# Optimization experiments

Hardware: AMD Instinct MI355X
Metric: run time of the kernel (lower is better)

## Reference

```python
import jax, jax.numpy as jnp
import numpy as np

B, C, H, W = 8, 256, 128, 128


def setup_inputs() -> dict:
    key = jax.random.key(0)
    k1, k2, k3, k4, k5 = jax.random.split(key, 5)
    x = jax.random.normal(k1, (B, C, H, W), dtype=jnp.float32)
    # 1x1 conv weights stored as (out_channels, in_channels); bias (out_channels,)
    w1 = jax.random.normal(k2, (C, C), dtype=jnp.float32) * (1.0 / np.sqrt(C))
    b1 = jax.random.normal(k3, (C,), dtype=jnp.float32) * 0.01
    w2 = jax.random.normal(k4, (C, C), dtype=jnp.float32) * (1.0 / np.sqrt(C))
    b2 = jax.random.normal(k5, (C,), dtype=jnp.float32) * 0.01
    return {"x": x, "w1": w1, "b1": b1, "w2": w2, "b2": b2}


def reference(x, w1, b1, w2, b2):
    b, c, h, w = x.shape
    xf = x.reshape(b, c, h * w)                      # (B, C, N)
    # 1x1 convs == per-pixel linear maps over channels
    q = jnp.einsum('oc,bcn->bon', w1, xf) + b1[None, :, None]   # (B, C, N)
    k = jnp.einsum('oc,bcn->bon', w2, xf) + b2[None, :, None]   # (B, C, N)
    # channel-attention Gram matrix: (B, C, N) @ (B, N, C) -> (B, C, C)
    attention = jnp.einsum('bcn,bdn->bcd', q, k)
    attention = jax.nn.softmax(attention, axis=-1)
    # (B, C, C) @ (B, C, N) -> (B, C, N), v = x itself (unprojected)
    attention_v = jnp.einsum('bcd,bdn->bcn', attention, xf).reshape(b, c, h, w)
    return x + attention_v
```

## Files before the change

### kernel.cpp

```cpp
#include <hip/hip_runtime.h>
#include <hip/hip_bf16.h>

#define B_    8
#define C_    256
#define NPIX  16384
#define BK    64
#define KC4   16
#define KCH4  (NPIX / KC4)
#define NSTEP4 (KCH4 / BK)

typedef __attribute__((ext_vector_type(8))) short bf16x8;
typedef __attribute__((ext_vector_type(4))) float f32x4;
typedef unsigned int uint_;

__device__ __forceinline__ unsigned short f2bf(float x) {
  unsigned int u = __builtin_bit_cast(unsigned int, x);
  u = (u + 0x7fffu + ((u >> 16) & 1u)) >> 16;
  return (unsigned short)u;
}
__device__ __forceinline__ float fcomp(const float4& v, int i) {
  switch (i) { case 0: return v.x; case 1: return v.y; case 2: return v.z; default: return v.w; }
}

template<bool XBF>
__global__ __launch_bounds__(512, 2) void k_gram(const float* __restrict__ x,
                                                 float* __restrict__ gpart,
                                                 float* __restrict__ spart,
                                                 unsigned short* __restrict__ xbf) {
  const int bid  = blockIdx.x;
  const int half = bid >> 7;
  const int b    = (bid >> 4) & 7;
  const int kc   = bid & 15;
  const float* X = x + (size_t)b * C_ * NPIX + kc * KCH4;

  __shared__ __align__(16) unsigned short Hi[2][256 * 64];
  __shared__ __align__(16) unsigned short Lo[2][256 * 64];

  const int tid  = threadIdx.x;
  const int lane = tid & 63;
  const int w    = tid >> 6;
  const int wr   = w >> 2;
  const int wc   = w & 3;

  const int srow = tid >> 4;
  const int scol = (tid & 15) * 4;
  const float* sp = X + (size_t)srow * NPIX + scol;
  unsigned short* xrow = XBF ?
      (xbf + (size_t)b * C_ * NPIX + (size_t)srow * NPIX + kc * KCH4 + scol) : nullptr;

  float rs[8] = {};
  float4 g[8];

#define GLOAD(ks)                                                             \
  _Pragma("unroll")                                                           \
  for (int j = 0; j < 8; ++j)                                                 \
    g[j] = *reinterpret_cast<const float4*>(sp + (size_t)j * 32 * NPIX + (ks) * BK);

#define STAGE(buf, ksn)                                                       \
  _Pragma("unroll")                                                           \
  for (int j = 0; j < 8; ++j) {                                               \
    const float4 v = g[j];                                                    \
    rs[j] += (v.x + v.y) + (v.z + v.w);                                       \
    const uint_ u0 = __builtin_bit_cast(uint_, v.x);                          \
    const uint_ u1 = __builtin_bit_cast(uint_, v.y);                          \
    const uint_ u2 = __builtin_bit_cast(uint_, v.z);                          \
    const uint_ u3 = __builtin_bit_cast(uint_, v.w);                          \
    uint2 hi, lo;                                                             \
    hi.x = (u0 >> 16) | (u1 & 0xffff0000u);                                   \
    hi.y = (u2 >> 16) | (u3 & 0xffff0000u);                                   \
    const float h0 = __builtin_bit_cast(float, u0 & 0xffff0000u);             \
    const float h1 = __builtin_bit_cast(float, u1 & 0xffff0000u);             \
    const float h2 = __builtin_bit_cast(float, u2 & 0xffff0000u);             \
    const float h3 = __builtin_bit_cast(float, u3 & 0xffff0000u);             \
    const uint_ l0 = __builtin_bit_cast(uint_, v.x - h0);                     \
    const uint_ l1 = __builtin_bit_cast(uint_, v.y - h1);                     \
    const uint_ l2 = __builtin_bit_cast(uint_, v.z - h2);                     \
    const uint_ l3 = __builtin_bit_cast(uint_, v.w - h3);                     \
    lo.x = (l0 >> 16) | (l1 & 0xffff0000u);                                   \
    lo.y = (l2 >> 16) | (l3 & 0xffff0000u);                                   \
    const int row = j * 32 + srow;                                            \
    const int idx = (row * 64 + scol) ^ ((row & 7) << 3);                     \
    *reinterpret_cast<uint2*>(&Hi[buf][idx]) = hi;                            \
    *reinterpret_cast<uint2*>(&Lo[buf][idx]) = lo;                            \
    if (XBF && (j >> 2) == half)                                              \
      *reinterpret_cast<uint2*>(xrow + (size_t)j * 32 * NPIX + (ksn) * BK) = hi; \
  }

  GLOAD(0)
  STAGE(0, 0)
  __syncthreads();

  f32x4 acc[4][4] = {};

  for (int ks = 0; ks < NSTEP4; ++ks) {
    const int cur = ks & 1;
    if (ks + 1 < NSTEP4) GLOAD(ks + 1)
    __builtin_amdgcn_s_setprio(1);
#pragma unroll
    for (int kk = 0; kk < 2; ++kk) {
      const int kb = kk * 32 + (lane >> 4) * 8;
      bf16x8 ahi[4], bhi[4], blo[4];
#pragma unroll
      for (int m = 0; m < 4; ++m) {
        const int row = half * 128 + wr * 64 + m * 16 + (lane & 15);
        ahi[m] = *reinterpret_cast<const bf16x8*>(&Hi[cur][(row * 64 + kb) ^ ((row & 7) << 3)]);
      }
#pragma unroll
      for (int n = 0; n < 4; ++n) {
        const int row = wc * 64 + n * 16 + (lane & 15);
        bhi[n] = *reinterpret_cast<const bf16x8*>(&Hi[cur][(row * 64 + kb) ^ ((row & 7) << 3)]);
      }
#pragma unroll
      for (int m = 0; m < 4; ++m)
#pragma unroll
        for (int n = 0; n < 4; ++n)
          acc[m][n] = __builtin_amdgcn_mfma_f32_16x16x32_bf16(ahi[m], bhi[n], acc[m][n], 0, 0, 0);
#pragma unroll
      for (int n = 0; n < 4; ++n) {
        const int row = wc * 64 + n * 16 + (lane & 15);
        blo[n] = *reinterpret_cast<const bf16x8*>(&Lo[cur][(row * 64 + kb) ^ ((row & 7) << 3)]);
      }
#pragma unroll
      for (int m = 0; m < 4; ++m)
#pragma unroll
        for (int n = 0; n < 4; ++n)
          acc[m][n] = __builtin_amdgcn_mfma_f32_16x16x32_bf16(ahi[m], blo[n], acc[m][n], 0, 0, 0);
#pragma unroll
      for (int m = 0; m < 4; ++m) {
        const int row = half * 128 + wr * 64 + m * 16 + (lane & 15);
        bf16x8 alo = *reinterpret_cast<const bf16x8*>(&Lo[cur][(row * 64 + kb) ^ ((row & 7) << 3)]);
#pragma unroll
        for (int n = 0; n < 4; ++n)
          acc[m][n] = __builtin_amdgcn_mfma_f32_16x16x32_bf16(alo, bhi[n], acc[m][n], 0, 0, 0);
      }
    }
    __builtin_amdgcn_s_setprio(0);
    if (ks + 1 < NSTEP4) STAGE(cur ^ 1, ks + 1)
    __syncthreads();
  }
#undef GLOAD
#undef STAGE

#pragma unroll
  for (int j = 0; j < 8; ++j) {
#pragma unroll
    for (int off = 1; off < 16; off <<= 1) rs[j] += __shfl_xor(rs[j], off, 64);
  }
  if (half == 0 && (tid & 15) == 0) {
#pragma unroll
    for (int j = 0; j < 8; ++j)
      spart[((size_t)b * KC4 + kc) * 256 + j * 32 + srow] = rs[j];
  }

  float* gp = gpart + (size_t)bid * (128 * 256);
#pragma unroll
  for (int m = 0; m < 4; ++m) {
    const int row0 = wr * 64 + m * 16 + ((lane >> 4) << 2);
#pragma unroll
    for (int n = 0; n < 4; ++n) {
      const int col = wc * 64 + n * 16 + (lane & 15);
#pragma unroll
      for (int j = 0; j < 4; ++j)
        gp[(size_t)(row0 + j) * 256 + col] = acc[m][n][j];
    }
  }
}

__global__ __launch_bounds__(256) void k_reduce(const float* __restrict__ gpart,
                                                float* __restrict__ G) {
  const int t  = blockIdx.x * 256 + threadIdx.x;
  const int b  = t >> 14;
  const int i  = (t >> 6) & 255;
  const int j4 = (t & 63) * 4;
  const int hb = (i >> 7) * 128 + b * 16;
  const int il = i & 127;
  float4 s = make_float4(0.f, 0.f, 0.f, 0.f);
#pragma unroll
  for (int kc = 0; kc < KC4; ++kc) {
    const float4 v = *reinterpret_cast<const float4*>(
        &gpart[(size_t)(hb + kc) * (128 * 256) + (size_t)il * 256 + j4]);
    s.x += v.x; s.y += v.y; s.z += v.z; s.w += v.w;
  }
  *reinterpret_cast<float4*>(&G[((size_t)b * 256 + i) * 256 + j4]) = s;
}

__global__ __launch_bounds__(256) void k_transpose(const float* __restrict__ in,
                                                   float* __restrict__ outp) {
  __shared__ float t[32][33];
  const int bx = blockIdx.x & 7, by = blockIdx.x >> 3;
  const int tx = threadIdx.x & 31, ty = threadIdx.x >> 5;
#pragma unroll
  for (int i = 0; i < 32; i += 8)
    t[ty + i][tx] = in[(size_t)(by * 32 + ty + i) * 256 + bx * 32 + tx];
  __syncthreads();
#pragma unroll
  for (int i = 0; i < 32; i += 8)
    outp[(size_t)(bx * 32 + ty + i) * 256 + by * 32 + tx] = t[tx][ty + i];
}

__global__ __launch_bounds__(256) void k_u(const float* __restrict__ w1,
                                           const float* __restrict__ w2,
                                           const float* __restrict__ spart,
                                           float* __restrict__ u1,
                                           float* __restrict__ u2) {
  const int b = blockIdx.x;
  const int tid = threadIdx.x;
  __shared__ float sl[256];
  float sv = 0.f;
#pragma unroll
  for (int kc = 0; kc < KC4; ++kc) sv += spart[((size_t)b * KC4 + kc) * 256 + tid];
  sl[tid] = sv;
  __syncthreads();
  float a1 = 0.f, a2 = 0.f;
#pragma unroll 4
  for (int c = 0; c < 256; ++c) {
    a1 += w1[(size_t)tid * 256 + c] * sl[c];
    a2 += w2[(size_t)tid * 256 + c] * sl[c];
  }
  u1[b * 256 + tid] = a1;
  u2[b * 256 + tid] = a2;
}

__global__ __launch_bounds__(256) void k_smallmm(const float* __restrict__ A, long asb,
                                                 const float* __restrict__ Bm, long bsb,
                                                 float* __restrict__ Cm, long csb) {
  const int b  = blockIdx.y;
  const int i0 = blockIdx.x * 8;
  const float* Ab = A  + (size_t)asb * b;
  const float* Bb = Bm + (size_t)bsb * b;
  float*       Cb = Cm + (size_t)csb * b;
  const int tid = threadIdx.x;
  __shared__ float arows[8][256];
#pragma unroll
  for (int rr = 0; rr < 8; ++rr) arows[rr][tid] = Ab[(size_t)(i0 + rr) * 256 + tid];
  __syncthreads();
  float acc[8] = {};
#pragma unroll 4
  for (int k = 0; k < 256; ++k) {
    const float bv = Bb[(size_t)k * 256 + tid];
#pragma unroll
    for (int rr = 0; rr < 8; ++rr) acc[rr] += arows[rr][k] * bv;
  }
#pragma unroll
  for (int rr = 0; rr < 8; ++rr) Cb[(size_t)(i0 + rr) * 256 + tid] = acc[rr];
}

__global__ __launch_bounds__(256) void k_softmax(const float* __restrict__ L,
                                                 const float* __restrict__ b1,
                                                 const float* __restrict__ b2,
                                                 const float* __restrict__ u1,
                                                 const float* __restrict__ u2,
                                                 unsigned short* __restrict__ Abf) {
  const int b = blockIdx.y, i = blockIdx.x, j = threadIdx.x;
  const size_t base = ((size_t)b * 256 + i) * 256;
  const float v = L[base + j] + u1[b * 256 + i] * b2[j] +
                  b1[i] * (u2[b * 256 + j] + 16384.f * b2[j]);
  const int lane = j & 63, wv = j >> 6;
  __shared__ float redm[4], reds[4];
  float m = v;
#pragma unroll
  for (int off = 32; off; off >>= 1) m = fmaxf(m, __shfl_xor(m, off, 64));
  if (lane == 0) redm[wv] = m;
  __syncthreads();
  m = fmaxf(fmaxf(redm[0], redm[1]), fmaxf(redm[2], redm[3]));
  const float e = __expf(v - m);
  float sm = e;
#pragma unroll
  for (int off = 32; off; off >>= 1) sm += __shfl_xor(sm, off, 64);
  if (lane == 0) reds[wv] = sm;
  __syncthreads();
  sm = (reds[0] + reds[1]) + (reds[2] + reds[3]);
  float p = e / sm;
  if (j == i) p += 1.0f;
  Abf[base + j] = f2bf(p);
}

template<bool XBF>
__global__ __launch_bounds__(256, 4) void k_av(const unsigned short* __restrict__ Abf,
                                               const float* __restrict__ x,
                                               const unsigned short* __restrict__ xbf,
                                               float* __restrict__ out) {
  const int bid = blockIdx.x;
  const int b = bid & 7;
  const int nbase = (bid >> 3) * 32;
  const unsigned short* Ab = Abf + (size_t)b * 65536;
  float* Ob = out + (size_t)b * C_ * NPIX;

  __shared__ __align__(16) unsigned short Xt[32 * 256];

  const int tid = threadIdx.x;
  const int lane = tid & 63, w = tid >> 6;

  if (XBF) {
    const unsigned short* Xh = xbf + (size_t)b * C_ * NPIX;
    const int pq = (tid & 7) * 4;
    const int dq = (tid >> 3) * 4;
#pragma unroll
    for (int h = 0; h < 2; ++h) {
      const int d = dq + h * 128;
      const unsigned short* xs = Xh + (size_t)d * NPIX + nbase + pq;
      ushort4 r0 = *reinterpret_cast<const ushort4*>(xs);
      ushort4 r1 = *reinterpret_cast<const ushort4*>(xs + NPIX);
      ushort4 r2 = *reinterpret_cast<const ushort4*>(xs + 2 * NPIX);
      ushort4 r3 = *reinterpret_cast<const ushort4*>(xs + 3 * NPIX);
      const ushort4 rr[4] = {r0, r1, r2, r3};
#pragma unroll
      for (int i = 0; i < 4; ++i) {
        const int px = pq + i;
        ushort4 v = make_ushort4(((const unsigned short*)&rr[0])[i],
                                 ((const unsigned short*)&rr[1])[i],
                                 ((const unsigned short*)&rr[2])[i],
                                 ((const unsigned short*)&rr[3])[i]);
        const int idx = (px * 256 + d) ^ (((px ^ (px >> 2)) & 7) << 3);
        *reinterpret_cast<ushort4*>(&Xt[idx]) = v;
      }
    }
  } else {
    const float* Xb = x + (size_t)b * C_ * NPIX;
    const int pq = (tid & 7) * 4;
    const int dq = (tid >> 3) * 4;
#pragma unroll
    for (int h = 0; h < 2; ++h) {
      const int d = dq + h * 128;
      const float* xs = Xb + (size_t)d * NPIX + nbase + pq;
      const float4 r0 = *reinterpret_cast<const float4*>(xs);
      const float4 r1 = *reinterpret_cast<const float4*>(xs + NPIX);
      const float4 r2 = *reinterpret_cast<const float4*>(xs + 2 * NPIX);
      const float4 r3 = *reinterpret_cast<const float4*>(xs + 3 * NPIX);
#pragma unroll
      for (int i = 0; i < 4; ++i) {
        const int px = pq + i;
        ushort4 v = make_ushort4(f2bf(fcomp(r0, i)), f2bf(fcomp(r1, i)),
                                 f2bf(fcomp(r2, i)), f2bf(fcomp(r3, i)));
        const int idx = (px * 256 + d) ^ (((px ^ (px >> 2)) & 7) << 3);
        *reinterpret_cast<ushort4*>(&Xt[idx]) = v;
      }
    }
  }
  __syncthreads();

  const int kboff = (lane >> 4) * 8;
  f32x4 acc[4][2] = {};
  bf16x8 afA[4], afB[4], bq[2];

#define LOADA(kk, af)                                                         \
  _Pragma("unroll")                                                           \
  for (int m = 0; m < 4; ++m)                                                 \
    af[m] = *reinterpret_cast<const bf16x8*>(                                 \
        Ab + (size_t)(w * 64 + m * 16 + (lane & 15)) * 256 + (kk) * 32 + kboff);

#define LOADB(kk)                                                             \
  _Pragma("unroll")                                                           \
  for (int n = 0; n < 2; ++n) {                                               \
    const int px = n * 16 + (lane & 15);                                      \
    bq[n] = *reinterpret_cast<const bf16x8*>(                                 \
        &Xt[(px * 256 + (kk) * 32 + kboff) ^ (((px ^ (px >> 2)) & 7) << 3)]); \
  }

#define MFMA8(af)                                                             \
  _Pragma("unroll")                                                           \
  for (int m = 0; m < 4; ++m)                                                 \
    _Pragma("unroll")                                                         \
    for (int n = 0; n < 2; ++n)                                               \
      acc[m][n] = __builtin_amdgcn_mfma_f32_16x16x32_bf16(bq[n], af[m], acc[m][n], 0, 0, 0);

  LOADA(0, afA)
#pragma unroll
  for (int kk = 0; kk < 8; ++kk) {
    LOADB(kk)
    if (kk < 7) {
      if (kk & 1) { LOADA(kk + 1, afA) } else { LOADA(kk + 1, afB) }
    }
    if (kk & 1) { MFMA8(afB) } else { MFMA8(afA) }
  }
#undef LOADA
#undef LOADB
#undef MFMA8

#pragma unroll
  for (int m = 0; m < 4; ++m) {
    const int ch = w * 64 + m * 16 + (lane & 15);
    float* orow = Ob + (size_t)ch * NPIX + nbase;
#pragma unroll
    for (int n = 0; n < 2; ++n) {
      const int p0 = n * 16 + ((lane >> 4) << 2);
      *reinterpret_cast<float4*>(orow + p0) = *reinterpret_cast<const float4*>(&acc[m][n]);
    }
  }
}

extern "C" void kernel_launch(void* const* d_in, const int* in_sizes, int n_in,
                              void* d_out, int out_size, void* d_ws, size_t ws_size,
                              hipStream_t stream) {
  const float* x  = (const float*)d_in[0];
  const float* w1 = (const float*)d_in[1];
  const float* b1 = (const float*)d_in[2];
  const float* w2 = (const float*)d_in[3];
  const float* b2 = (const float*)d_in[4];
  float* out = (float*)d_out;
  char* ws = (char*)d_ws;

  float* gpart = out;

  constexpr size_t G_OFF     = 0;
  constexpr size_t T1_OFF    = G_OFF   + (size_t)B_ * C_ * C_ * 4;
  constexpr size_t L_OFF     = T1_OFF  + (size_t)B_ * C_ * C_ * 4;
  constexpr size_t W2T_OFF   = L_OFF   + (size_t)B_ * C_ * C_ * 4;
  constexpr size_t SPART_OFF = W2T_OFF + (size_t)C_ * C_ * 4;
  constexpr size_t U1_OFF    = SPART_OFF + (size_t)B_ * KC4 * C_ * 4;
  constexpr size_t U2_OFF    = U1_OFF  + (size_t)B_ * C_ * 4;
  constexpr size_t ABF_OFF   = U2_OFF  + (size_t)B_ * C_ * 4;
  constexpr size_t XBF_OFF   = ABF_OFF + (size_t)B_ * C_ * C_ * 2;
  constexpr size_t XBF_BYTES = (size_t)B_ * C_ * NPIX * 2;

  float* G     = (float*)(ws + G_OFF);
  float* T1    = (float*)(ws + T1_OFF);
  float* Lb    = (float*)(ws + L_OFF);
  float* w2t   = (float*)(ws + W2T_OFF);
  float* spart = (float*)(ws + SPART_OFF);
  float* u1    = (float*)(ws + U1_OFF);
  float* u2    = (float*)(ws + U2_OFF);
  unsigned short* Abf = (unsigned short*)(ws + ABF_OFF);
  unsigned short* Xbf = (unsigned short*)(ws + XBF_OFF);

  const bool xbf_ok = ws_size >= XBF_OFF + XBF_BYTES;

  k_transpose<<<64, 256, 0, stream>>>(w2, w2t);
  if (xbf_ok) k_gram<true> <<<256, 512, 0, stream>>>(x, gpart, spart, Xbf);
  else        k_gram<false><<<256, 512, 0, stream>>>(x, gpart, spart, nullptr);
  k_reduce   <<<512, 256, 0, stream>>>(gpart, G);
  k_u        <<<B_, 256, 0, stream>>>(w1, w2, spart, u1, u2);
  k_smallmm  <<<dim3(32, B_), 256, 0, stream>>>(w1, 0, G, C_ * C_, T1, C_ * C_);
  k_smallmm  <<<dim3(32, B_), 256, 0, stream>>>(T1, C_ * C_, w2t, 0, Lb, C_ * C_);
  k_softmax  <<<dim3(C_, B_), 256, 0, stream>>>(Lb, b1, b2, u1, u2, Abf);
  if (xbf_ok) k_av<true> <<<4096, 256, 0, stream>>>(Abf, x, Xbf, out);
  else        k_av<false><<<4096, 256, 0, stream>>>(Abf, x, nullptr, out);
}
```

Before: 220.5 us.

## Split Gram K-dimension into 32 chunks and single-buffer LDS staging

Doubles the number of K-chunks in the Gram kernel, so the grid grows from 256 to 512 blocks and the per-block LDS shrinks from double-buffered to single-buffered. Staging now happens at the top of each iteration behind a barrier, with the next global load issued before the MFMA work. The goal is to fill more CUs and lift occupancy on a chip with 256 CUs. The cost is twice as many partial Gram tiles written and reduced, and less overlap between LDS staging and compute.

After: 254.9 us. 15.6% more time.

```diff
diff --git a/kernel.cpp b/kernel.cpp
--- a/kernel.cpp
+++ b/kernel.cpp
@@ -5,9 +5,9 @@
 #define C_    256
 #define NPIX  16384
 #define BK    64
-#define KC4   16
-#define KCH4  (NPIX / KC4)
-#define NSTEP4 (KCH4 / BK)
+#define KCG   32
+#define KCHG  (NPIX / KCG)
+#define NSTEPG (KCHG / BK)
 
 typedef __attribute__((ext_vector_type(8))) short bf16x8;
 typedef __attribute__((ext_vector_type(4))) float f32x4;
@@ -23,18 +23,18 @@
 }
 
 template<bool XBF>
-__global__ __launch_bounds__(512, 2) void k_gram(const float* __restrict__ x,
-                                                 float* __restrict__ gpart,
-                                                 float* __restrict__ spart,
-                                                 unsigned short* __restrict__ xbf) {
+__global__ __launch_bounds__(512) void k_gram(const float* __restrict__ x,
+                                              float* __restrict__ gpart,
+                                              float* __restrict__ spart,
+                                              unsigned short* __restrict__ xbf) {
   const int bid  = blockIdx.x;
-  const int half = bid >> 7;
-  const int b    = (bid >> 4) & 7;
-  const int kc   = bid & 15;
-  const float* X = x + (size_t)b * C_ * NPIX + kc * KCH4;
-
-  __shared__ __align__(16) unsigned short Hi[2][256 * 64];
-  __shared__ __align__(16) unsigned short Lo[2][256 * 64];
+  const int half = bid >> 8;
+  const int b    = (bid >> 5) & 7;
+  const int kc   = bid & 31;
+  const float* X = x + (size_t)b * C_ * NPIX + kc * KCHG;
+
+  __shared__ __align__(16) unsigned short Hi[256 * 64];
+  __shared__ __align__(16) unsigned short Lo[256 * 64];
 
   const int tid  = threadIdx.x;
   const int lane = tid & 63;
@@ -46,7 +46,7 @@
   const int scol = (tid & 15) * 4;
   const float* sp = X + (size_t)srow * NPIX + scol;
   unsigned short* xrow = XBF ?
-      (xbf + (size_t)b * C_ * NPIX + (size_t)srow * NPIX + kc * KCH4 + scol) : nullptr;
+      (xbf + (size_t)b * C_ * NPIX + (size_t)srow * NPIX + kc * KCHG + scol) : nullptr;
 
   float rs[8] = {};
   float4 g[8];
@@ -56,7 +56,7 @@
   for (int j = 0; j < 8; ++j)                                                 \
     g[j] = *reinterpret_cast<const float4*>(sp + (size_t)j * 32 * NPIX + (ks) * BK);
 
-#define STAGE(buf, ksn)                                                       \
+#define STAGE(ksn)                                                            \
   _Pragma("unroll")                                                           \
   for (int j = 0; j < 8; ++j) {                                               \
     const float4 v = g[j];                                                    \
@@ -80,21 +80,20 @@
     lo.y = (l2 >> 16) | (l3 & 0xffff0000u);                                   \
     const int row = j * 32 + srow;                                            \
     const int idx = (row * 64 + scol) ^ ((row & 7) << 3);                     \
-    *reinterpret_cast<uint2*>(&Hi[buf][idx]) = hi;                            \
-    *reinterpret_cast<uint2*>(&Lo[buf][idx]) = lo;                            \
+    *reinterpret_cast<uint2*>(&Hi[idx]) = hi;                                 \
+    *reinterpret_cast<uint2*>(&Lo[idx]) = lo;                                 \
     if (XBF && (j >> 2) == half)                                              \
       *reinterpret_cast<uint2*>(xrow + (size_t)j * 32 * NPIX + (ksn) * BK) = hi; \
   }
 
   GLOAD(0)
-  STAGE(0, 0)
-  __syncthreads();
 
   f32x4 acc[4][4] = {};
 
-  for (int ks = 0; ks < NSTEP4; ++ks) {
-    const int cur = ks & 1;
-    if (ks + 1 < NSTEP4) GLOAD(ks + 1)
+  for (int ks = 0; ks < NSTEPG; ++ks) {
+    STAGE(ks)
+    __syncthreads();
+    if (ks + 1 < NSTEPG) GLOAD(ks + 1)
     __builtin_amdgcn_s_setprio(1);
 #pragma unroll
     for (int kk = 0; kk < 2; ++kk) {
@@ -103,12 +102,12 @@
 #pragma unroll
       for (int m = 0; m < 4; ++m) {
         const int row = half * 128 + wr * 64 + m * 16 + (lane & 15);
-        ahi[m] = *reinterpret_cast<const bf16x8*>(&Hi[cur][(row * 64 + kb) ^ ((row & 7) << 3)]);
+        ahi[m] = *reinterpret_cast<const bf16x8*>(&Hi[(row * 64 + kb) ^ ((row & 7) << 3)]);
       }
 #pragma unroll
       for (int n = 0; n < 4; ++n) {
         const int row = wc * 64 + n * 16 + (lane & 15);
-        bhi[n] = *reinterpret_cast<const bf16x8*>(&Hi[cur][(row * 64 + kb) ^ ((row & 7) << 3)]);
+        bhi[n] = *reinterpret_cast<const bf16x8*>(&Hi[(row * 64 + kb) ^ ((row & 7) << 3)]);
       }
 #pragma unroll
       for (int m = 0; m < 4; ++m)
@@ -118,7 +117,7 @@
 #pragma unroll
       for (int n = 0; n < 4; ++n) {
         const int row = wc * 64 + n * 16 + (lane & 15);
-        blo[n] = *reinterpret_cast<const bf16x8*>(&Lo[cur][(row * 64 + kb) ^ ((row & 7) << 3)]);
+        blo[n] = *reinterpret_cast<const bf16x8*>(&Lo[(row * 64 + kb) ^ ((row & 7) << 3)]);
       }
 #pragma unroll
       for (int m = 0; m < 4; ++m)
@@ -128,14 +127,13 @@
 #pragma unroll
       for (int m = 0; m < 4; ++m) {
         const int row = half * 128 + wr * 64 + m * 16 + (lane & 15);
-        bf16x8 alo = *reinterpret_cast<const bf16x8*>(&Lo[cur][(row * 64 + kb) ^ ((row & 7) << 3)]);
+        bf16x8 alo = *reinterpret_cast<const bf16x8*>(&Lo[(row * 64 + kb) ^ ((row & 7) << 3)]);
 #pragma unroll
         for (int n = 0; n < 4; ++n)
           acc[m][n] = __builtin_amdgcn_mfma_f32_16x16x32_bf16(alo, bhi[n], acc[m][n], 0, 0, 0);
       }
     }
     __builtin_amdgcn_s_setprio(0);
-    if (ks + 1 < NSTEP4) STAGE(cur ^ 1, ks + 1)
     __syncthreads();
   }
 #undef GLOAD
@@ -149,7 +147,7 @@
   if (half == 0 && (tid & 15) == 0) {
 #pragma unroll
     for (int j = 0; j < 8; ++j)
-      spart[((size_t)b * KC4 + kc) * 256 + j * 32 + srow] = rs[j];
+      spart[((size_t)b * KCG + kc) * 256 + j * 32 + srow] = rs[j];
   }
 
   float* gp = gpart + (size_t)bid * (128 * 256);
@@ -172,11 +170,11 @@
   const int b  = t >> 14;
   const int i  = (t >> 6) & 255;
   const int j4 = (t & 63) * 4;
-  const int hb = (i >> 7) * 128 + b * 16;
+  const int hb = (i >> 7) * 256 + b * 32;
   const int il = i & 127;
   float4 s = make_float4(0.f, 0.f, 0.f, 0.f);
 #pragma unroll
-  for (int kc = 0; kc < KC4; ++kc) {
+  for (int kc = 0; kc < KCG; ++kc) {
     const float4 v = *reinterpret_cast<const float4*>(
         &gpart[(size_t)(hb + kc) * (128 * 256) + (size_t)il * 256 + j4]);
     s.x += v.x; s.y += v.y; s.z += v.z; s.w += v.w;
@@ -208,7 +206,7 @@
   __shared__ float sl[256];
   float sv = 0.f;
 #pragma unroll
-  for (int kc = 0; kc < KC4; ++kc) sv += spart[((size_t)b * KC4 + kc) * 256 + tid];
+  for (int kc = 0; kc < KCG; ++kc) sv += spart[((size_t)b * KCG + kc) * 256 + tid];
   sl[tid] = sv;
   __syncthreads();
   float a1 = 0.f, a2 = 0.f;
@@ -407,7 +405,7 @@
   constexpr size_t L_OFF     = T1_OFF  + (size_t)B_ * C_ * C_ * 4;
   constexpr size_t W2T_OFF   = L_OFF   + (size_t)B_ * C_ * C_ * 4;
   constexpr size_t SPART_OFF = W2T_OFF + (size_t)C_ * C_ * 4;
-  constexpr size_t U1_OFF    = SPART_OFF + (size_t)B_ * KC4 * C_ * 4;
+  constexpr size_t U1_OFF    = SPART_OFF + (size_t)B_ * KCG * C_ * 4;
   constexpr size_t U2_OFF    = U1_OFF  + (size_t)B_ * C_ * 4;
   constexpr size_t ABF_OFF   = U2_OFF  + (size_t)B_ * C_ * 4;
   constexpr size_t XBF_OFF   = ABF_OFF + (size_t)B_ * C_ * C_ * 2;
@@ -426,8 +424,8 @@
   const bool xbf_ok = ws_size >= XBF_OFF + XBF_BYTES;
 
   k_transpose<<<64, 256, 0, stream>>>(w2, w2t);
-  if (xbf_ok) k_gram<true> <<<256, 512, 0, stream>>>(x, gpart, spart, Xbf);
-  else        k_gram<false><<<256, 512, 0, stream>>>(x, gpart, spart, nullptr);
+  if (xbf_ok) k_gram<true> <<<512, 512, 0, stream>>>(x, gpart, spart, Xbf);
+  else        k_gram<false><<<512, 512, 0, stream>>>(x, gpart, spart, nullptr);
   k_reduce   <<<512, 256, 0, stream>>>(gpart, G);
   k_u        <<<B_, 256, 0, stream>>>(w1, w2, spart, u1, u2);
   k_smallmm  <<<dim3(32, B_), 256, 0, stream>>>(w1, 0, G, C_ * C_, T1, C_ * C_);
```

## Make k_av persistent over four pixel tiles with double-buffered LDS prefetch

Applied to the files above, without the earlier changes.

Each k_av block now handles four 32-pixel tiles instead of one, so the grid shrinks from 4096 to 1024 blocks. The next tile's X values are prefetched from global into registers while MFMAs run on the current tile, using a double-buffered LDS transpose. MFMA sections are wrapped in s_setprio. This is meant to hide global load latency and cut per-block launch overhead, at the cost of more registers (the occupancy hint in launch_bounds is dropped), double the LDS, and fewer blocks to spread across CUs.

Result: slower. 225.9 us (+2.5%).

```diff
diff --git a/kernel.cpp b/kernel.cpp
--- a/kernel.cpp
+++ b/kernel.cpp
@@ -276,72 +276,70 @@
 }
 
 template<bool XBF>
-__global__ __launch_bounds__(256, 4) void k_av(const unsigned short* __restrict__ Abf,
-                                               const float* __restrict__ x,
-                                               const unsigned short* __restrict__ xbf,
-                                               float* __restrict__ out) {
+__global__ __launch_bounds__(256) void k_av(const unsigned short* __restrict__ Abf,
+                                            const float* __restrict__ x,
+                                            const unsigned short* __restrict__ xbf,
+                                            float* __restrict__ out) {
   const int bid = blockIdx.x;
   const int b = bid & 7;
-  const int nbase = (bid >> 3) * 32;
+  const int pxbase = (bid >> 3) * 128;
   const unsigned short* Ab = Abf + (size_t)b * 65536;
   float* Ob = out + (size_t)b * C_ * NPIX;
 
-  __shared__ __align__(16) unsigned short Xt[32 * 256];
+  __shared__ __align__(16) unsigned short Xt[2][32 * 256];
 
   const int tid = threadIdx.x;
   const int lane = tid & 63, w = tid >> 6;
-
-  if (XBF) {
-    const unsigned short* Xh = xbf + (size_t)b * C_ * NPIX;
-    const int pq = (tid & 7) * 4;
-    const int dq = (tid >> 3) * 4;
-#pragma unroll
-    for (int h = 0; h < 2; ++h) {
-      const int d = dq + h * 128;
-      const unsigned short* xs = Xh + (size_t)d * NPIX + nbase + pq;
-      ushort4 r0 = *reinterpret_cast<const ushort4*>(xs);
-      ushort4 r1 = *reinterpret_cast<const ushort4*>(xs + NPIX);
-      ushort4 r2 = *reinterpret_cast<const ushort4*>(xs + 2 * NPIX);
-      ushort4 r3 = *reinterpret_cast<const ushort4*>(xs + 3 * NPIX);
-      const ushort4 rr[4] = {r0, r1, r2, r3};
-#pragma unroll
-      for (int i = 0; i < 4; ++i) {
-        const int px = pq + i;
-        ushort4 v = make_ushort4(((const unsigned short*)&rr[0])[i],
-                                 ((const unsigned short*)&rr[1])[i],
-                                 ((const unsigned short*)&rr[2])[i],
-                                 ((const unsigned short*)&rr[3])[i]);
-        const int idx = (px * 256 + d) ^ (((px ^ (px >> 2)) & 7) << 3);
-        *reinterpret_cast<ushort4*>(&Xt[idx]) = v;
-      }
-    }
-  } else {
-    const float* Xb = x + (size_t)b * C_ * NPIX;
-    const int pq = (tid & 7) * 4;
-    const int dq = (tid >> 3) * 4;
-#pragma unroll
-    for (int h = 0; h < 2; ++h) {
-      const int d = dq + h * 128;
-      const float* xs = Xb + (size_t)d * NPIX + nbase + pq;
-      const float4 r0 = *reinterpret_cast<const float4*>(xs);
-      const float4 r1 = *reinterpret_cast<const float4*>(xs + NPIX);
-      const float4 r2 = *reinterpret_cast<const float4*>(xs + 2 * NPIX);
-      const float4 r3 = *reinterpret_cast<const float4*>(xs + 3 * NPIX);
-#pragma unroll
-      for (int i = 0; i < 4; ++i) {
-        const int px = pq + i;
-        ushort4 v = make_ushort4(f2bf(fcomp(r0, i)), f2bf(fcomp(r1, i)),
-                                 f2bf(fcomp(r2, i)), f2bf(fcomp(r3, i)));
-        const int idx = (px * 256 + d) ^ (((px ^ (px >> 2)) & 7) << 3);
-        *reinterpret_cast<ushort4*>(&Xt[idx]) = v;
-      }
-    }
-  }
-  __syncthreads();
-
+  const int pq = (tid & 7) * 4;
+  const int dq = (tid >> 3) * 4;
   const int kboff = (lane >> 4) * 8;
-  f32x4 acc[4][2] = {};
-  bf16x8 afA[4], afB[4], bq[2];
+
+  const unsigned short* Xh = XBF ? (xbf + (size_t)b * C_ * NPIX) : nullptr;
+  const float*          Xf = XBF ? nullptr : (x + (size_t)b * C_ * NPIX);
+
+  ushort4 gbh[8];
+  float4  gbf[8];
+
+#define GLD(t)                                                                \
+  if (XBF) {                                                                  \
+    _Pragma("unroll")                                                         \
+    for (int h = 0; h < 2; ++h)                                               \
+      _Pragma("unroll")                                                       \
+      for (int r = 0; r < 4; ++r)                                             \
+        gbh[h * 4 + r] = *reinterpret_cast<const ushort4*>(                   \
+            Xh + (size_t)(dq + h * 128 + r) * NPIX + pxbase + (t) * 32 + pq); \
+  } else {                                                                    \
+    _Pragma("unroll")                                                         \
+    for (int h = 0; h < 2; ++h)                                               \
+      _Pragma("unroll")                                                       \
+      for (int r = 0; r < 4; ++r)                                             \
+        gbf[h * 4 + r] = *reinterpret_cast<const float4*>(                    \
+            Xf + (size_t)(dq + h * 128 + r) * NPIX + pxbase + (t) * 32 + pq); \
+  }
+
+#define CONV(buf)                                                             \
+  _Pragma("unroll")                                                           \
+  for (int h = 0; h < 2; ++h) {                                               \
+    const int d = dq + h * 128;                                               \
+    _Pragma("unroll")                                                         \
+    for (int i = 0; i < 4; ++i) {                                             \
+      const int px = pq + i;                                                  \
+      ushort4 v;                                                              \
+      if (XBF) {                                                              \
+        v = make_ushort4(((const unsigned short*)&gbh[h * 4 + 0])[i],         \
+                         ((const unsigned short*)&gbh[h * 4 + 1])[i],         \
+                         ((const unsigned short*)&gbh[h * 4 + 2])[i],         \
+                         ((const unsigned short*)&gbh[h * 4 + 3])[i]);        \
+      } else {                                                                \
+        v = make_ushort4(f2bf(fcomp(gbf[h * 4 + 0], i)),                      \
+                         f2bf(fcomp(gbf[h * 4 + 1], i)),                      \
+                         f2bf(fcomp(gbf[h * 4 + 2], i)),                      \
+                         f2bf(fcomp(gbf[h * 4 + 3], i)));                     \
+      }                                                                       \
+      const int idx = (px * 256 + d) ^ (((px ^ (px >> 2)) & 7) << 3);         \
+      *reinterpret_cast<ushort4*>(&Xt[buf][idx]) = v;                         \
+    }                                                                         \
+  }
 
 #define LOADA(kk, af)                                                         \
   _Pragma("unroll")                                                           \
@@ -349,12 +347,12 @@
     af[m] = *reinterpret_cast<const bf16x8*>(                                 \
         Ab + (size_t)(w * 64 + m * 16 + (lane & 15)) * 256 + (kk) * 32 + kboff);
 
-#define LOADB(kk)                                                             \
+#define LOADB(kk, buf)                                                        \
   _Pragma("unroll")                                                           \
   for (int n = 0; n < 2; ++n) {                                               \
     const int px = n * 16 + (lane & 15);                                      \
     bq[n] = *reinterpret_cast<const bf16x8*>(                                 \
-        &Xt[(px * 256 + (kk) * 32 + kboff) ^ (((px ^ (px >> 2)) & 7) << 3)]); \
+        &Xt[buf][(px * 256 + (kk) * 32 + kboff) ^ (((px ^ (px >> 2)) & 7) << 3)]); \
   }
 
 #define MFMA8(af)                                                             \
@@ -364,29 +362,45 @@
     for (int n = 0; n < 2; ++n)                                               \
       acc[m][n] = __builtin_amdgcn_mfma_f32_16x16x32_bf16(bq[n], af[m], acc[m][n], 0, 0, 0);
 
-  LOADA(0, afA)
-#pragma unroll
-  for (int kk = 0; kk < 8; ++kk) {
-    LOADB(kk)
-    if (kk < 7) {
-      if (kk & 1) { LOADA(kk + 1, afA) } else { LOADA(kk + 1, afB) }
+  GLD(0)
+#pragma unroll
+  for (int t = 0; t < 4; ++t) {
+    const int buf = t & 1;
+    CONV(buf)
+    __syncthreads();
+
+    bf16x8 afA[4], afB[4], bq[2];
+    LOADA(0, afA)
+    if (t < 3) GLD(t + 1)
+
+    f32x4 acc[4][2] = {};
+    __builtin_amdgcn_s_setprio(1);
+#pragma unroll
+    for (int kk = 0; kk < 8; ++kk) {
+      LOADB(kk, buf)
+      if (kk < 7) {
+        if (kk & 1) { LOADA(kk + 1, afA) } else { LOADA(kk + 1, afB) }
+      }
+      if (kk & 1) { MFMA8(afB) } else { MFMA8(afA) }
     }
-    if (kk & 1) { MFMA8(afB) } else { MFMA8(afA) }
-  }
+    __builtin_amdgcn_s_setprio(0);
+
+#pragma unroll
+    for (int m = 0; m < 4; ++m) {
+      const int ch = w * 64 + m * 16 + (lane & 15);
+      float* orow = Ob + (size_t)ch * NPIX + pxbase + t * 32;
+#pragma unroll
+      for (int n = 0; n < 2; ++n) {
+        const int p0 = n * 16 + ((lane >> 4) << 2);
+        *reinterpret_cast<float4*>(orow + p0) = *reinterpret_cast<const float4*>(&acc[m][n]);
+      }
+    }
+  }
+#undef GLD
+#undef CONV
 #undef LOADA
 #undef LOADB
 #undef MFMA8
-
-#pragma unroll
-  for (int m = 0; m < 4; ++m) {
-    const int ch = w * 64 + m * 16 + (lane & 15);
-    float* orow = Ob + (size_t)ch * NPIX + nbase;
-#pragma unroll
-    for (int n = 0; n < 2; ++n) {
-      const int p0 = n * 16 + ((lane >> 4) << 2);
-      *reinterpret_cast<float4*>(orow + p0) = *reinterpret_cast<const float4*>(&acc[m][n]);
-    }
-  }
 }
 
 extern "C" void kernel_launch(void* const* d_in, const int* in_sizes, int n_in,
@@ -433,6 +447,6 @@
   k_smallmm  <<<dim3(32, B_), 256, 0, stream>>>(w1, 0, G, C_ * C_, T1, C_ * C_);
   k_smallmm  <<<dim3(32, B_), 256, 0, stream>>>(T1, C_ * C_, w2t, 0, Lb, C_ * C_);
   k_softmax  <<<dim3(C_, B_), 256, 0, stream>>>(Lb, b1, b2, u1, u2, Abf);
-  if (xbf_ok) k_av<true> <<<4096, 256, 0, stream>>>(Abf, x, Xbf, out);
-  else        k_av<false><<<4096, 256, 0, stream>>>(Abf, x, nullptr, out);
-}
+  if (xbf_ok) k_av<true> <<<1024, 256, 0, stream>>>(Abf, x, Xbf, out);
+  else        k_av<false><<<1024, 256, 0, stream>>>(Abf, x, nullptr, out);
+}
```
